# Optimization experiments

Measured on AMD Instinct MI355X. Metric: run time of the kernel, lower is better.

## Reference

```python
import jax, jax.numpy as jnp
import numpy as np

DIM = 1024
HEADS = 16
DK = DIM // HEADS
B, LQ, LKV = 2, 2048, 2048


def setup_inputs() -> dict:
    key = jax.random.key(0)
    ks = jax.random.split(key, 12)
    s = 1.0 / np.sqrt(DIM)
    return {
        "output": jax.random.normal(ks[0], (B, LQ, DIM), jnp.float32),
        "context": jax.random.normal(ks[1], (B, LKV, DIM), jnp.float32),
        # torch nn.Linear(dim, dim): store as [in, out] so y = x @ W + b
        "Wq": jax.random.normal(ks[2], (DIM, DIM), jnp.float32) * s,
        "bq": jax.random.normal(ks[3], (DIM,), jnp.float32) * s,
        "Wk": jax.random.normal(ks[4], (DIM, DIM), jnp.float32) * s,
        "bk": jax.random.normal(ks[5], (DIM,), jnp.float32) * s,
        "Wv": jax.random.normal(ks[6], (DIM, DIM), jnp.float32) * s,
        "bv": jax.random.normal(ks[7], (DIM,), jnp.float32) * s,
        # linear_out: in = 2*dim, out = dim
        "Wo": jax.random.normal(ks[8], (2 * DIM, DIM), jnp.float32) * (1.0 / np.sqrt(2 * DIM)),
        "bo": jax.random.normal(ks[9], (DIM,), jnp.float32) * (1.0 / np.sqrt(2 * DIM)),
    }


def _to_batches(x):
    # [B, L, dim] -> [B*H, L, dk], same layout as the torch reshape/permute
    b, l, _ = x.shape
    return x.reshape(b, l, HEADS, DK).transpose(0, 2, 1, 3).reshape(b * HEADS, l, DK)


def reference(output, context, Wq, bq, Wk, bk, Wv, bv, Wo, bo):
    b, lq, dim = output.shape
    q = _to_batches(output @ Wq + bq)     # [B*H, Lq, dk]
    k = _to_batches(context @ Wk + bk)    # [B*H, Lkv, dk]
    v = _to_batches(context @ Wv + bv)    # [B*H, Lkv, dk]

    scores = jnp.einsum('bqd,bkd->bqk', q, k) / jnp.sqrt(jnp.asarray(DK, q.dtype))
    attn = jax.nn.softmax(scores, axis=-1)            # [B*H, Lq, Lkv]; dropout = identity at eval
    ctx = jnp.einsum('bqk,bkd->bqd', attn, v)          # [B*H, Lq, dk]

    # Faithful to the original (non-standard) reshape:
    # scores.transpose(1,2).contiguous().view(B, -1, dim)
    concat = ctx.transpose(0, 2, 1).reshape(b, -1, dim)  # [B, Lq, dim] (permuted layout)
    combined = jnp.concatenate([concat, output], axis=2)  # [B, Lq, 2*dim]
    out = jnp.tanh(combined @ Wo + bo)                     # [B, Lq, dim]
    return (out, attn)
```

## Files before the change

### kernel.cpp

```cpp
#include <hip/hip_runtime.h>
#include <math.h>
#include <stdint.h>

#define DIM_ 1024
#define HEADS_ 16
#define DK_ 64
#define B_ 2
#define L_ 2048
#define BH_ (B_*HEADS_)
#define M_ (B_*L_)

typedef __attribute__((ext_vector_type(4))) float f32x4;
typedef __attribute__((ext_vector_type(8))) short bf16x8;
typedef __attribute__((ext_vector_type(4))) short bf16x4;

#define QSCALE 0.18033688f

static __device__ __forceinline__ short f2bf(float f) {
    uint32_t u = __builtin_bit_cast(uint32_t, f);
    u += 0x7fffu + ((u >> 16) & 1u);
    return (short)(u >> 16);
}
static __device__ __forceinline__ void gload16(const void* g, void* l) {
    __builtin_amdgcn_global_load_lds(
        (const __attribute__((address_space(1))) unsigned int*)g,
        (__attribute__((address_space(3))) unsigned int*)l, 16, 0, 0);
}

__global__ __launch_bounds__(256)
void prep(const float* __restrict__ xout, const float* __restrict__ xctx,
          const float* __restrict__ Wq, const float* __restrict__ Wk,
          const float* __restrict__ Wv, const float* __restrict__ Wo,
          short* __restrict__ xoutb, short* __restrict__ xctxb,
          short* __restrict__ WqT, short* __restrict__ WkT,
          short* __restrict__ WvT, short* __restrict__ WoT)
{
    __shared__ float ts[64][65];
    const int bid = blockIdx.x;
    const int tid = threadIdx.x;
    if (bid < 4096) {
        const int id = bid * 256 + tid;
        const int nA = (M_ * DIM_) / 8;
        const float* src = (id < nA) ? xout : xctx;
        short* dst = (id < nA) ? xoutb : xctxb;
        const int c = (id < nA) ? id : id - nA;
        const f32x4 v0 = *(const f32x4*)&src[(size_t)c * 8];
        const f32x4 v1 = *(const f32x4*)&src[(size_t)c * 8 + 4];
        bf16x8 o;
#pragma unroll
        for (int i = 0; i < 4; ++i) { o[i] = f2bf(v0[i]); o[4 + i] = f2bf(v1[i]); }
        *(bf16x8*)&dst[(size_t)c * 8] = o;
        return;
    }
    const int flat = bid - 4096;
    const int z = flat >> 9;
    const int rem = flat & 511;
    const int K = (z == 3) ? 2 * DIM_ : DIM_;
    const int k0 = (rem & 31) * 64;
    if (k0 >= K) return;
    const int n0 = (rem >> 5) * 64;
    const float* W = (z == 0) ? Wq : (z == 1) ? Wk : (z == 2) ? Wv : Wo;
    short* WT = (z == 0) ? WqT : (z == 1) ? WkT : (z == 2) ? WvT : WoT;
    {
        const int k = tid >> 2, noff = (tid & 3) * 16;
#pragma unroll
        for (int i = 0; i < 4; ++i)
            *(f32x4*)&ts[k][noff + i * 4] =
                *(const f32x4*)&W[(size_t)(k0 + k) * DIM_ + n0 + noff + i * 4];
    }
    __syncthreads();
    {
        const int n = tid >> 2, koff = (tid & 3) * 16;
#pragma unroll
        for (int c = 0; c < 2; ++c) {
            bf16x8 o;
#pragma unroll
            for (int i = 0; i < 8; ++i) o[i] = f2bf(ts[koff + c * 8 + i][n]);
            *(bf16x8*)&WT[(size_t)(n0 + n) * K + k0 + koff + c * 8] = o;
        }
    }
}

__global__ __launch_bounds__(256)
void qkv_mfma(const short* __restrict__ xoutb, const short* __restrict__ xctxb,
              const short* __restrict__ WqT, const short* __restrict__ WkT,
              const short* __restrict__ WvT,
              const float* __restrict__ bq, const float* __restrict__ bk,
              const float* __restrict__ bv,
              short* __restrict__ qh, short* __restrict__ kh, short* __restrict__ vT)
{
    const int z = blockIdx.z;
    const short* A  = (z == 0) ? xoutb : xctxb;
    const short* Bt = (z == 0) ? WqT : (z == 1) ? WkT : WvT;
    const float* bias = (z == 0) ? bq : (z == 1) ? bk : bv;

    const int flat = blockIdx.y * 8 + blockIdx.x;
    const int wgs = (flat & 7) * 32 + (flat >> 3);
    const int col0 = (wgs & 7) * 128;
    const int row0 = (wgs >> 3) * 128;
    const int tid = threadIdx.x;
    const int lane = tid & 63;
    const int w = tid >> 6;
    const int wm = (w >> 1) * 64, wn = (w & 1) * 64;
    const int l15 = lane & 15, g = lane >> 4;
    const int sub = lane >> 3, slt = lane & 7;

    __shared__ short As[128 * 64];
    __shared__ short Bs[128 * 64];

    const short* pA[4]; const short* pB[4]; short* ldsA[4]; short* ldsB[4];
#pragma unroll
    for (int i = 0; i < 4; ++i) {
        const int r = w * 32 + i * 8 + sub;
        const int sc = ((slt ^ (r & 7)) * 8);
        pA[i] = A  + (size_t)(row0 + r) * DIM_ + sc;
        pB[i] = Bt + (size_t)(col0 + r) * DIM_ + sc;
        ldsA[i] = &As[(w * 32 + i * 8) * 64];
        ldsB[i] = &Bs[(w * 32 + i * 8) * 64];
    }

    f32x4 acc[4][4];
#pragma unroll
    for (int mi = 0; mi < 4; ++mi)
#pragma unroll
        for (int ni = 0; ni < 4; ++ni) acc[mi][ni] = (f32x4)0.f;

    for (int k0 = 0; k0 < DIM_; k0 += 64) {
#pragma unroll
        for (int i = 0; i < 4; ++i) {
            gload16(pA[i] + k0, ldsA[i]);
            gload16(pB[i] + k0, ldsB[i]);
        }
        __syncthreads();
        bf16x8 af[4][2], bfr[4][2];
#pragma unroll
        for (int mi = 0; mi < 4; ++mi) {
            const int wa = wm + mi * 16 + l15;
#pragma unroll
            for (int ks = 0; ks < 2; ++ks)
                af[mi][ks] = *(const bf16x8*)&As[wa * 64 + (((ks * 4 + g) ^ (wa & 7)) * 8)];
        }
#pragma unroll
        for (int ni = 0; ni < 4; ++ni) {
            const int wb = wn + ni * 16 + l15;
#pragma unroll
            for (int ks = 0; ks < 2; ++ks)
                bfr[ni][ks] = *(const bf16x8*)&Bs[wb * 64 + (((ks * 4 + g) ^ (wb & 7)) * 8)];
        }
        __builtin_amdgcn_s_setprio(1);
#pragma unroll
        for (int mi = 0; mi < 4; ++mi)
#pragma unroll
            for (int ni = 0; ni < 4; ++ni)
#pragma unroll
                for (int ks = 0; ks < 2; ++ks)
                    acc[mi][ni] = __builtin_amdgcn_mfma_f32_16x16x32_bf16(af[mi][ks], bfr[ni][ks], acc[mi][ni], 0, 0, 0);
        __builtin_amdgcn_s_setprio(0);
        __syncthreads();
    }

#pragma unroll
    for (int ni = 0; ni < 4; ++ni) {
        const int col = col0 + wn + ni * 16 + l15;
        const int h = col >> 6, dk = col & 63;
        const float bb = bias[col];
#pragma unroll
        for (int mi = 0; mi < 4; ++mi) {
            const int rowb = row0 + wm + mi * 16 + g * 4;
            const int b = rowb >> 11;
            const int l = rowb & (L_ - 1);
            const int bh = b * 16 + h;
            if (z == 2) {
                bf16x4 o;
#pragma unroll
                for (int r = 0; r < 4; ++r) o[r] = f2bf(acc[mi][ni][r] + bb);
                *(bf16x4*)&vT[(size_t)(bh * 64 + dk) * L_ + l] = o;
            } else {
                short* dst = (z == 0) ? qh : kh;
                const float sc = (z == 0) ? QSCALE : 1.0f;
#pragma unroll
                for (int r = 0; r < 4; ++r)
                    dst[((size_t)bh * L_ + l + r) * DK_ + dk] = f2bf((acc[mi][ni][r] + bb) * sc);
            }
        }
    }
}

__global__ __launch_bounds__(512, 8)
void attn_mfma(const short* __restrict__ qh, const short* __restrict__ kh,
               const short* __restrict__ vT,
               float* __restrict__ attn, short* __restrict__ ctxTb)
{
    const int bid = blockIdx.x;
    const int wg = (bid & 7) * 128 + (bid >> 3);
    const int bh = wg >> 5;
    const int q0 = (wg & 31) * 64;

    const int tid = threadIdx.x;
    const int lane = tid & 63;
    const int w = tid >> 6;
    const int wq = w >> 1, wk = w & 1;
    const int l15 = lane & 15, g = lane >> 4;

    __shared__ short SM[17408];
    short* const Kb0 = SM;
    short* const Kb1 = SM + 4096;
    short* const Vb  = SM + 8192;
    short* const Psb = SM + 12288;
    float* const stat = (float*)(SM + 16896);

    const short* kbase = kh + (size_t)bh * (L_ * DK_);
    const short* vbase = vT + (size_t)bh * (DK_ * L_);

    const int lr = lane >> 3, ls = lane & 7;
    const int srow = w * 8 + lr;
    const short* kSrc = kbase + (size_t)srow * DK_ + ((ls ^ (srow & 7)) * 8);
    const short* vSrc = vbase + (size_t)srow * L_ + ((ls ^ (srow & 7)) * 8);

    bf16x8 qf[2];
#pragma unroll
    for (int ks = 0; ks < 2; ++ks)
        qf[ks] = *(const bf16x8*)&qh[((size_t)bh * L_ + q0 + wq * 16 + l15) * DK_ + ks * 32 + g * 8];

    int kbOff[2][2], vbOff[4];
#pragma unroll
    for (int cc = 0; cc < 2; ++cc)
#pragma unroll
        for (int ks = 0; ks < 2; ++ks) {
            const int row = wk * 32 + cc * 16 + l15;
            kbOff[cc][ks] = row * 64 + (((ks * 4 + g) ^ (row & 7)) * 8);
        }
#pragma unroll
    for (int nf = 0; nf < 4; ++nf) {
        const int row = nf * 16 + l15;
        vbOff[nf] = row * 64 + (((wk * 4 + g) ^ (row & 7)) * 8);
    }

    float m[4], s[4];
#pragma unroll
    for (int r = 0; r < 4; ++r) { m[r] = -1e30f; s[r] = 0.f; }

#pragma unroll
    for (int i = 0; i < 3; ++i)
        gload16(kSrc + (size_t)i * 64 * DK_, SM + (i << 12) + w * 512);
    asm volatile("s_waitcnt vmcnt(2)" ::: "memory");
    __builtin_amdgcn_sched_barrier(0);
    __builtin_amdgcn_s_barrier();

    for (int t = 0; t < 32; ++t) {
        if (t < 29)
            gload16(kSrc + (size_t)(t + 3) * 64 * DK_, SM + (((t + 3) & 3) << 12) + w * 512);
        const short* kb = SM + ((t & 3) << 12);
        f32x4 sa[2];
#pragma unroll
        for (int cc = 0; cc < 2; ++cc) sa[cc] = (f32x4)0.f;
        __builtin_amdgcn_s_setprio(1);
#pragma unroll
        for (int cc = 0; cc < 2; ++cc)
#pragma unroll
            for (int ks = 0; ks < 2; ++ks)
                sa[cc] = __builtin_amdgcn_mfma_f32_16x16x32_bf16(qf[ks], *(const bf16x8*)&kb[kbOff[cc][ks]], sa[cc], 0, 0, 0);
        __builtin_amdgcn_s_setprio(0);
#pragma unroll
        for (int r = 0; r < 4; ++r) {
            const float tm = fmaxf(sa[0][r], sa[1][r]);
            const float mn = fmaxf(m[r], tm);
            s[r] = s[r] * exp2f(m[r] - mn) + exp2f(sa[0][r] - mn) + exp2f(sa[1][r] - mn);
            m[r] = mn;
        }
        if (t < 29)       { asm volatile("s_waitcnt vmcnt(2)" ::: "memory"); }
        else if (t == 29) { asm volatile("s_waitcnt vmcnt(1)" ::: "memory"); }
        else if (t == 30) { asm volatile("s_waitcnt vmcnt(0)" ::: "memory"); }
        __builtin_amdgcn_sched_barrier(0);
        if (t < 31) __builtin_amdgcn_s_barrier();
    }
#pragma unroll
    for (int mask = 1; mask <= 8; mask <<= 1) {
#pragma unroll
        for (int r = 0; r < 4; ++r) {
            const float mo = __shfl_xor(m[r], mask);
            const float so = __shfl_xor(s[r], mask);
            const float mn = fmaxf(m[r], mo);
            s[r] = s[r] * exp2f(m[r] - mn) + so * exp2f(mo - mn);
            m[r] = mn;
        }
    }
    if (l15 == 0) {
#pragma unroll
        for (int r = 0; r < 4; ++r) {
            stat[((wq * 2 + wk) * 16 + g * 4 + r) * 2 + 0] = m[r];
            stat[((wq * 2 + wk) * 16 + g * 4 + r) * 2 + 1] = s[r];
        }
    }
    gload16(kSrc, SM + w * 512);
    asm volatile("s_waitcnt lgkmcnt(0)" ::: "memory");
    __builtin_amdgcn_s_barrier();
    float inv_s[4];
#pragma unroll
    for (int r = 0; r < 4; ++r) {
        const float m0 = stat[((wq * 2 + 0) * 16 + g * 4 + r) * 2 + 0];
        const float s0 = stat[((wq * 2 + 0) * 16 + g * 4 + r) * 2 + 1];
        const float m1 = stat[((wq * 2 + 1) * 16 + g * 4 + r) * 2 + 0];
        const float s1 = stat[((wq * 2 + 1) * 16 + g * 4 + r) * 2 + 1];
        const float mn = fmaxf(m0, m1);
        m[r] = mn;
        inv_s[r] = 1.0f / (s0 * exp2f(m0 - mn) + s1 * exp2f(m1 - mn));
    }

    f32x4 cacc[4];
#pragma unroll
    for (int nf = 0; nf < 4; ++nf) cacc[nf] = (f32x4)0.f;

    float* attnB = attn + ((size_t)bh * L_ + q0) * L_;

    asm volatile("s_waitcnt vmcnt(0)" ::: "memory");
    __builtin_amdgcn_sched_barrier(0);
    __builtin_amdgcn_s_barrier();

    for (int t = 0; t < 32; ++t) {
        if (t) {
            asm volatile("s_waitcnt vmcnt(8)" ::: "memory");
            __builtin_amdgcn_sched_barrier(0);
            __builtin_amdgcn_s_barrier();
        }
        gload16(vSrc + t * 64, Vb + w * 512);
        {
            const int tn = (t < 31) ? t + 1 : t;
            gload16(kSrc + (size_t)tn * 64 * DK_, ((t & 1) ? Kb0 : Kb1) + w * 512);
        }
        const short* kb = (t & 1) ? Kb1 : Kb0;
        f32x4 sa[2];
#pragma unroll
        for (int cc = 0; cc < 2; ++cc) sa[cc] = (f32x4)0.f;
        __builtin_amdgcn_s_setprio(1);
#pragma unroll
        for (int cc = 0; cc < 2; ++cc)
#pragma unroll
            for (int ks = 0; ks < 2; ++ks)
                sa[cc] = __builtin_amdgcn_mfma_f32_16x16x32_bf16(qf[ks], *(const bf16x8*)&kb[kbOff[cc][ks]], sa[cc], 0, 0, 0);
        __builtin_amdgcn_s_setprio(0);
#pragma unroll
        for (int cc = 0; cc < 2; ++cc)
#pragma unroll
            for (int r = 0; r < 4; ++r) {
                const float p = exp2f(sa[cc][r] - m[r]) * inv_s[r];
                Psb[(wq * 16 + g * 4 + r) * 72 + wk * 32 + cc * 16 + l15] = f2bf(p);
                __builtin_nontemporal_store(
                    p, attnB + (size_t)(wq * 16 + g * 4 + r) * L_ + t * 64 + wk * 32 + cc * 16 + l15);
            }
        asm volatile("s_waitcnt vmcnt(9) lgkmcnt(0)" ::: "memory");
        __builtin_amdgcn_sched_barrier(0);
        __builtin_amdgcn_s_barrier();
        const bf16x8 pa = *(const bf16x8*)&Psb[(wq * 16 + l15) * 72 + wk * 32 + g * 8];
        __builtin_amdgcn_s_setprio(1);
#pragma unroll
        for (int nf = 0; nf < 4; ++nf)
            cacc[nf] = __builtin_amdgcn_mfma_f32_16x16x32_bf16(pa, *(const bf16x8*)&Vb[vbOff[nf]], cacc[nf], 0, 0, 0);
        __builtin_amdgcn_s_setprio(0);
    }

    __syncthreads();
    float* scr = (float*)Kb0;
    float* scr1 = (float*)Kb1;
    if (wk) {
#pragma unroll
        for (int nf = 0; nf < 4; ++nf) {
            float* p = (nf < 2) ? scr : scr1;
            *(f32x4*)&p[(((wq * 2) + (nf & 1)) * 64 + lane) * 4] = cacc[nf];
        }
    }
    __syncthreads();
    if (!wk) {
#pragma unroll
        for (int nf = 0; nf < 4; ++nf) {
            const float* p = (nf < 2) ? scr : scr1;
            const f32x4 o = cacc[nf] + *(const f32x4*)&p[(((wq * 2) + (nf & 1)) * 64 + lane) * 4];
            bf16x4 ob;
#pragma unroll
            for (int r = 0; r < 4; ++r) ob[r] = f2bf(o[r]);
            *(bf16x4*)&ctxTb[(size_t)(bh * 64 + nf * 16 + l15) * L_ + q0 + wq * 16 + g * 4] = ob;
        }
    }
}

__global__ __launch_bounds__(256)
void out_mfma(const short* __restrict__ ctxTb, const short* __restrict__ xoutb,
              const short* __restrict__ WoT, const float* __restrict__ bo,
              float* __restrict__ out)
{
    const int flat = blockIdx.y * 16 + blockIdx.x;
    const int wgs = (flat & 7) * 64 + (flat >> 3);
    const int col0 = (wgs & 15) * 64;
    const int row0 = (wgs >> 4) * 128;
    const int tid = threadIdx.x;
    const int lane = tid & 63;
    const int w = tid >> 6;
    const int wm = (w >> 1) * 64, wn = (w & 1) * 32;
    const int l15 = lane & 15, g = lane >> 4;
    const int sub = lane >> 3, slt = lane & 7;

    __shared__ short As[128 * 64];
    __shared__ short Bs[64 * 64];

    const short* pA1[4]; const short* pA2[4]; const short* pB[2];
    short* ldsA[4]; short* ldsB[2];
#pragma unroll
    for (int i = 0; i < 4; ++i) {
        const int r = w * 32 + i * 8 + sub;
        const int rr = row0 + r;
        const int b = rr >> 11, l_ = rr & (L_ - 1);
        const int bh = b * 16 + (l_ >> 7), d = (l_ & 127) >> 1;
        const size_t off1 = ((size_t)(bh * 64 + d) << 11) + (size_t)((l_ & 1) << 10);
        const int sc = ((slt ^ (r & 7)) * 8);
        pA1[i] = ctxTb + off1 + sc;
        pA2[i] = xoutb + (size_t)rr * DIM_ + sc;
        ldsA[i] = &As[(w * 32 + i * 8) * 64];
    }
#pragma unroll
    for (int i = 0; i < 2; ++i) {
        const int r = w * 16 + i * 8 + sub;
        const int sc = ((slt ^ (r & 7)) * 8);
        pB[i]  = WoT + (size_t)(col0 + r) * (2 * DIM_) + sc;
        ldsB[i] = &Bs[(w * 16 + i * 8) * 64];
    }

    f32x4 acc[4][2];
#pragma unroll
    for (int mi = 0; mi < 4; ++mi)
#pragma unroll
        for (int ni = 0; ni < 2; ++ni) acc[mi][ni] = (f32x4)0.f;

    for (int k0 = 0; k0 < 2 * DIM_; k0 += 64) {
        const bool first = (k0 < DIM_);
        const int kk = first ? k0 : k0 - DIM_;
#pragma unroll
        for (int i = 0; i < 4; ++i)
            gload16(first ? (pA1[i] + kk) : (pA2[i] + kk), ldsA[i]);
#pragma unroll
        for (int i = 0; i < 2; ++i)
            gload16(pB[i] + k0, ldsB[i]);
        __syncthreads();
        bf16x8 af[4][2], bfr[2][2];
#pragma unroll
        for (int mi = 0; mi < 4; ++mi) {
            const int wa = wm + mi * 16 + l15;
#pragma unroll
            for (int ks = 0; ks < 2; ++ks)
                af[mi][ks] = *(const bf16x8*)&As[wa * 64 + (((ks * 4 + g) ^ (wa & 7)) * 8)];
        }
#pragma unroll
        for (int ni = 0; ni < 2; ++ni) {
            const int wb = wn + ni * 16 + l15;
#pragma unroll
            for (int ks = 0; ks < 2; ++ks)
                bfr[ni][ks] = *(const bf16x8*)&Bs[wb * 64 + (((ks * 4 + g) ^ (wb & 7)) * 8)];
        }
        __builtin_amdgcn_s_setprio(1);
#pragma unroll
        for (int mi = 0; mi < 4; ++mi)
#pragma unroll
            for (int ni = 0; ni < 2; ++ni)
#pragma unroll
                for (int ks = 0; ks < 2; ++ks)
                    acc[mi][ni] = __builtin_amdgcn_mfma_f32_16x16x32_bf16(af[mi][ks], bfr[ni][ks], acc[mi][ni], 0, 0, 0);
        __builtin_amdgcn_s_setprio(0);
        __syncthreads();
    }

#pragma unroll
    for (int ni = 0; ni < 2; ++ni) {
        const int col = col0 + wn + ni * 16 + l15;
        const float bb = bo[col];
#pragma unroll
        for (int mi = 0; mi < 4; ++mi) {
            const int rowb = row0 + wm + mi * 16 + g * 4;
#pragma unroll
            for (int r = 0; r < 4; ++r)
                out[(size_t)(rowb + r) * DIM_ + col] = tanhf(acc[mi][ni][r] + bb);
        }
    }
}

extern "C" void kernel_launch(void* const* d_in, const int* in_sizes, int n_in,
                              void* d_out, int out_size, void* d_ws, size_t ws_size,
                              hipStream_t stream)
{
    const float* xout = (const float*)d_in[0];
    const float* xctx = (const float*)d_in[1];
    const float* Wq = (const float*)d_in[2];
    const float* bq = (const float*)d_in[3];
    const float* Wk = (const float*)d_in[4];
    const float* bk = (const float*)d_in[5];
    const float* Wv = (const float*)d_in[6];
    const float* bv = (const float*)d_in[7];
    const float* Wo = (const float*)d_in[8];
    const float* bo = (const float*)d_in[9];

    float* out  = (float*)d_out;
    float* attn = out + (size_t)M_ * DIM_;

    short* ws = (short*)d_ws;
    short* xoutb = ws;
    short* xctxb = xoutb + (size_t)M_ * DIM_;
    short* WqT   = xctxb + (size_t)M_ * DIM_;
    short* WkT   = WqT + (size_t)DIM_ * DIM_;
    short* WvT   = WkT + (size_t)DIM_ * DIM_;
    short* WoT   = WvT + (size_t)DIM_ * DIM_;
    short* qh    = WoT + (size_t)2 * DIM_ * DIM_;
    short* kh    = qh + (size_t)BH_ * L_ * DK_;
    short* vT    = kh + (size_t)BH_ * L_ * DK_;
    short* ctxTb = vT + (size_t)BH_ * L_ * DK_;

    prep<<<6144, 256, 0, stream>>>(xout, xctx, Wq, Wk, Wv, Wo,
                                   xoutb, xctxb, WqT, WkT, WvT, WoT);
    qkv_mfma<<<dim3(8, 32, 3), 256, 0, stream>>>(
        xoutb, xctxb, WqT, WkT, WvT, bq, bk, bv, qh, kh, vT);
    attn_mfma<<<1024, 512, 0, stream>>>(qh, kh, vT, attn, ctxTb);
    out_mfma<<<dim3(16, 32), 256, 0, stream>>>(ctxTb, xoutb, WoT, bo, out);
}
```

Measured before the change: 279.2 us.

## Process two K tiles per barrier and lazily rescale softmax running max

The softmax statistics pass now handles two 64-row K tiles per loop iteration and loads the next pair together, which halves the number of workgroup barriers and waitcnt points. The running max is only updated, with its exp2 rescale of the sum, when some lane's tile max exceeds the current max by more than 8 in the log2 domain. Otherwise the new exponentials are added straight to the sum. The re-prefetch of the first K tile is moved after the barrier that follows the stat writes. The trade-off is a shorter effective prefetch distance, because each iteration waits on vmcnt(0) for the pair it just issued, plus a wave-wide vote branch in the inner loop.

```diff
diff --git a/kernel.cpp b/kernel.cpp
--- a/kernel.cpp
+++ b/kernel.cpp
@@ -241,38 +241,58 @@
     for (int r = 0; r < 4; ++r) { m[r] = -1e30f; s[r] = 0.f; }
 
 #pragma unroll
-    for (int i = 0; i < 3; ++i)
+    for (int i = 0; i < 4; ++i)
         gload16(kSrc + (size_t)i * 64 * DK_, SM + (i << 12) + w * 512);
     asm volatile("s_waitcnt vmcnt(2)" ::: "memory");
     __builtin_amdgcn_sched_barrier(0);
     __builtin_amdgcn_s_barrier();
 
-    for (int t = 0; t < 32; ++t) {
-        if (t < 29)
-            gload16(kSrc + (size_t)(t + 3) * 64 * DK_, SM + (((t + 3) & 3) << 12) + w * 512);
-        const short* kb = SM + ((t & 3) << 12);
-        f32x4 sa[2];
-#pragma unroll
-        for (int cc = 0; cc < 2; ++cc) sa[cc] = (f32x4)0.f;
-        __builtin_amdgcn_s_setprio(1);
-#pragma unroll
-        for (int cc = 0; cc < 2; ++cc)
-#pragma unroll
-            for (int ks = 0; ks < 2; ++ks)
-                sa[cc] = __builtin_amdgcn_mfma_f32_16x16x32_bf16(qf[ks], *(const bf16x8*)&kb[kbOff[cc][ks]], sa[cc], 0, 0, 0);
-        __builtin_amdgcn_s_setprio(0);
-#pragma unroll
-        for (int r = 0; r < 4; ++r) {
-            const float tm = fmaxf(sa[0][r], sa[1][r]);
-            const float mn = fmaxf(m[r], tm);
-            s[r] = s[r] * exp2f(m[r] - mn) + exp2f(sa[0][r] - mn) + exp2f(sa[1][r] - mn);
-            m[r] = mn;
-        }
-        if (t < 29)       { asm volatile("s_waitcnt vmcnt(2)" ::: "memory"); }
-        else if (t == 29) { asm volatile("s_waitcnt vmcnt(1)" ::: "memory"); }
-        else if (t == 30) { asm volatile("s_waitcnt vmcnt(0)" ::: "memory"); }
-        __builtin_amdgcn_sched_barrier(0);
-        if (t < 31) __builtin_amdgcn_s_barrier();
+    for (int j = 0; j < 16; ++j) {
+        if (j >= 1 && j < 15) {
+            const size_t t2 = (size_t)(2 * j + 2);
+            gload16(kSrc + t2 * 64 * DK_, SM + (((2 * j + 2) & 3) << 12) + w * 512);
+            gload16(kSrc + (t2 + 1) * 64 * DK_, SM + (((2 * j + 3) & 3) << 12) + w * 512);
+        }
+        f32x4 sa[2][2];
+#pragma unroll
+        for (int u = 0; u < 2; ++u) {
+            const short* kb = SM + (((2 * j + u) & 3) << 12);
+            sa[u][0] = (f32x4)0.f; sa[u][1] = (f32x4)0.f;
+            __builtin_amdgcn_s_setprio(1);
+#pragma unroll
+            for (int cc = 0; cc < 2; ++cc)
+#pragma unroll
+                for (int ks = 0; ks < 2; ++ks)
+                    sa[u][cc] = __builtin_amdgcn_mfma_f32_16x16x32_bf16(qf[ks], *(const bf16x8*)&kb[kbOff[cc][ks]], sa[u][cc], 0, 0, 0);
+            __builtin_amdgcn_s_setprio(0);
+        }
+#pragma unroll
+        for (int u = 0; u < 2; ++u) {
+            float tm[4];
+            bool need = false;
+#pragma unroll
+            for (int r = 0; r < 4; ++r) {
+                tm[r] = fmaxf(sa[u][0][r], sa[u][1][r]);
+                need |= (tm[r] > m[r] + 8.0f);
+            }
+            if (__any(need)) {
+#pragma unroll
+                for (int r = 0; r < 4; ++r) {
+                    const float mn = fmaxf(m[r], tm[r]);
+                    s[r] = s[r] * exp2f(m[r] - mn) + exp2f(sa[u][0][r] - mn) + exp2f(sa[u][1][r] - mn);
+                    m[r] = mn;
+                }
+            } else {
+#pragma unroll
+                for (int r = 0; r < 4; ++r)
+                    s[r] += exp2f(sa[u][0][r] - m[r]) + exp2f(sa[u][1][r] - m[r]);
+            }
+        }
+        if (j < 15) {
+            asm volatile("s_waitcnt vmcnt(0)" ::: "memory");
+            __builtin_amdgcn_sched_barrier(0);
+            __builtin_amdgcn_s_barrier();
+        }
     }
 #pragma unroll
     for (int mask = 1; mask <= 8; mask <<= 1) {
@@ -292,9 +312,9 @@
             stat[((wq * 2 + wk) * 16 + g * 4 + r) * 2 + 1] = s[r];
         }
     }
-    gload16(kSrc, SM + w * 512);
     asm volatile("s_waitcnt lgkmcnt(0)" ::: "memory");
     __builtin_amdgcn_s_barrier();
+    gload16(kSrc, SM + w * 512);
     float inv_s[4];
 #pragma unroll
     for (int r = 0; r < 4; ++r) {
```

Measured after the change: 284.6 us. About the same (+2.0%).

## Load K/V fragments directly from global into registers, dropping LDS staging and barriers

Applied to the files above, without the earlier changes.

The attention kernel no longer stages K and V tiles through shared memory with async global-to-LDS copies and block-wide barriers. Each wave now reads its own MFMA operand fragments straight from global memory into registers, with a two-deep register double buffer in the stats pass. The P tile exchange is kept wave-local, so the per-iteration s_barrier is removed and the occupancy hint in launch_bounds is relaxed. This trades barrier and LDS-copy overhead for redundant global or cache reads, since several waves now fetch the same K rows, and for higher register pressure and exposed load latency.

```diff
diff --git a/kernel.cpp b/kernel.cpp
--- a/kernel.cpp
+++ b/kernel.cpp
@@ -186,7 +186,7 @@
     }
 }
 
-__global__ __launch_bounds__(512, 8)
+__global__ __launch_bounds__(512)
 void attn_mfma(const short* __restrict__ qh, const short* __restrict__ kh,
                const short* __restrict__ vT,
                float* __restrict__ attn, short* __restrict__ ctxTb)
@@ -203,76 +203,87 @@
     const int l15 = lane & 15, g = lane >> 4;
 
     __shared__ short SM[17408];
-    short* const Kb0 = SM;
-    short* const Kb1 = SM + 4096;
-    short* const Vb  = SM + 8192;
     short* const Psb = SM + 12288;
     float* const stat = (float*)(SM + 16896);
 
     const short* kbase = kh + (size_t)bh * (L_ * DK_);
     const short* vbase = vT + (size_t)bh * (DK_ * L_);
 
-    const int lr = lane >> 3, ls = lane & 7;
-    const int srow = w * 8 + lr;
-    const short* kSrc = kbase + (size_t)srow * DK_ + ((ls ^ (srow & 7)) * 8);
-    const short* vSrc = vbase + (size_t)srow * L_ + ((ls ^ (srow & 7)) * 8);
-
     bf16x8 qf[2];
 #pragma unroll
     for (int ks = 0; ks < 2; ++ks)
         qf[ks] = *(const bf16x8*)&qh[((size_t)bh * L_ + q0 + wq * 16 + l15) * DK_ + ks * 32 + g * 8];
 
-    int kbOff[2][2], vbOff[4];
+    int kfOff[2][2], vfOff[4];
 #pragma unroll
     for (int cc = 0; cc < 2; ++cc)
 #pragma unroll
-        for (int ks = 0; ks < 2; ++ks) {
-            const int row = wk * 32 + cc * 16 + l15;
-            kbOff[cc][ks] = row * 64 + (((ks * 4 + g) ^ (row & 7)) * 8);
-        }
-#pragma unroll
-    for (int nf = 0; nf < 4; ++nf) {
-        const int row = nf * 16 + l15;
-        vbOff[nf] = row * 64 + (((wk * 4 + g) ^ (row & 7)) * 8);
-    }
+        for (int ks = 0; ks < 2; ++ks)
+            kfOff[cc][ks] = (wk * 32 + cc * 16 + l15) * 64 + ks * 32 + g * 8;
+#pragma unroll
+    for (int nf = 0; nf < 4; ++nf)
+        vfOff[nf] = (nf * 16 + l15) * L_ + wk * 32 + g * 8;
 
     float m[4], s[4];
 #pragma unroll
     for (int r = 0; r < 4; ++r) { m[r] = -1e30f; s[r] = 0.f; }
 
-#pragma unroll
-    for (int i = 0; i < 3; ++i)
-        gload16(kSrc + (size_t)i * 64 * DK_, SM + (i << 12) + w * 512);
-    asm volatile("s_waitcnt vmcnt(2)" ::: "memory");
-    __builtin_amdgcn_sched_barrier(0);
-    __builtin_amdgcn_s_barrier();
-
-    for (int t = 0; t < 32; ++t) {
-        if (t < 29)
-            gload16(kSrc + (size_t)(t + 3) * 64 * DK_, SM + (((t + 3) & 3) << 12) + w * 512);
-        const short* kb = SM + ((t & 3) << 12);
-        f32x4 sa[2];
-#pragma unroll
-        for (int cc = 0; cc < 2; ++cc) sa[cc] = (f32x4)0.f;
-        __builtin_amdgcn_s_setprio(1);
-#pragma unroll
-        for (int cc = 0; cc < 2; ++cc)
-#pragma unroll
-            for (int ks = 0; ks < 2; ++ks)
-                sa[cc] = __builtin_amdgcn_mfma_f32_16x16x32_bf16(qf[ks], *(const bf16x8*)&kb[kbOff[cc][ks]], sa[cc], 0, 0, 0);
-        __builtin_amdgcn_s_setprio(0);
-#pragma unroll
-        for (int r = 0; r < 4; ++r) {
-            const float tm = fmaxf(sa[0][r], sa[1][r]);
-            const float mn = fmaxf(m[r], tm);
-            s[r] = s[r] * exp2f(m[r] - mn) + exp2f(sa[0][r] - mn) + exp2f(sa[1][r] - mn);
-            m[r] = mn;
-        }
-        if (t < 29)       { asm volatile("s_waitcnt vmcnt(2)" ::: "memory"); }
-        else if (t == 29) { asm volatile("s_waitcnt vmcnt(1)" ::: "memory"); }
-        else if (t == 30) { asm volatile("s_waitcnt vmcnt(0)" ::: "memory"); }
-        __builtin_amdgcn_sched_barrier(0);
-        if (t < 31) __builtin_amdgcn_s_barrier();
+    bf16x8 kA[2][2], kB[2][2];
+#pragma unroll
+    for (int cc = 0; cc < 2; ++cc)
+#pragma unroll
+        for (int ks = 0; ks < 2; ++ks)
+            kA[cc][ks] = *(const bf16x8*)&kbase[kfOff[cc][ks]];
+
+    for (int t = 0; t < 32; t += 2) {
+        if (t + 1 < 32) {
+            const short* kt = kbase + (size_t)(t + 1) * 64 * DK_;
+#pragma unroll
+            for (int cc = 0; cc < 2; ++cc)
+#pragma unroll
+                for (int ks = 0; ks < 2; ++ks)
+                    kB[cc][ks] = *(const bf16x8*)&kt[kfOff[cc][ks]];
+        }
+        {
+            f32x4 sa0 = (f32x4)0.f, sa1 = (f32x4)0.f;
+            __builtin_amdgcn_s_setprio(1);
+            sa0 = __builtin_amdgcn_mfma_f32_16x16x32_bf16(qf[0], kA[0][0], sa0, 0, 0, 0);
+            sa0 = __builtin_amdgcn_mfma_f32_16x16x32_bf16(qf[1], kA[0][1], sa0, 0, 0, 0);
+            sa1 = __builtin_amdgcn_mfma_f32_16x16x32_bf16(qf[0], kA[1][0], sa1, 0, 0, 0);
+            sa1 = __builtin_amdgcn_mfma_f32_16x16x32_bf16(qf[1], kA[1][1], sa1, 0, 0, 0);
+            __builtin_amdgcn_s_setprio(0);
+#pragma unroll
+            for (int r = 0; r < 4; ++r) {
+                const float tm = fmaxf(sa0[r], sa1[r]);
+                const float mn = fmaxf(m[r], tm);
+                s[r] = s[r] * exp2f(m[r] - mn) + exp2f(sa0[r] - mn) + exp2f(sa1[r] - mn);
+                m[r] = mn;
+            }
+        }
+        if (t + 2 < 32) {
+            const short* kt = kbase + (size_t)(t + 2) * 64 * DK_;
+#pragma unroll
+            for (int cc = 0; cc < 2; ++cc)
+#pragma unroll
+                for (int ks = 0; ks < 2; ++ks)
+                    kA[cc][ks] = *(const bf16x8*)&kt[kfOff[cc][ks]];
+        }
+        {
+            f32x4 sa0 = (f32x4)0.f, sa1 = (f32x4)0.f;
+            __builtin_amdgcn_s_setprio(1);
+            sa0 = __builtin_amdgcn_mfma_f32_16x16x32_bf16(qf[0], kB[0][0], sa0, 0, 0, 0);
+            sa0 = __builtin_amdgcn_mfma_f32_16x16x32_bf16(qf[1], kB[0][1], sa0, 0, 0, 0);
+            sa1 = __builtin_amdgcn_mfma_f32_16x16x32_bf16(qf[0], kB[1][0], sa1, 0, 0, 0);
+            sa1 = __builtin_amdgcn_mfma_f32_16x16x32_bf16(qf[1], kB[1][1], sa1, 0, 0, 0);
+            __builtin_amdgcn_s_setprio(0);
+#pragma unroll
+            for (int r = 0; r < 4; ++r) {
+                const float tm = fmaxf(sa0[r], sa1[r]);
+                const float mn = fmaxf(m[r], tm);
+                s[r] = s[r] * exp2f(m[r] - mn) + exp2f(sa0[r] - mn) + exp2f(sa1[r] - mn);
+                m[r] = mn;
+            }
+        }
     }
 #pragma unroll
     for (int mask = 1; mask <= 8; mask <<= 1) {
@@ -292,9 +303,7 @@
             stat[((wq * 2 + wk) * 16 + g * 4 + r) * 2 + 1] = s[r];
         }
     }
-    gload16(kSrc, SM + w * 512);
-    asm volatile("s_waitcnt lgkmcnt(0)" ::: "memory");
-    __builtin_amdgcn_s_barrier();
+    __syncthreads();
     float inv_s[4];
 #pragma unroll
     for (int r = 0; r < 4; ++r) {
@@ -312,56 +321,54 @@
     for (int nf = 0; nf < 4; ++nf) cacc[nf] = (f32x4)0.f;
 
     float* attnB = attn + ((size_t)bh * L_ + q0) * L_;
-
-    asm volatile("s_waitcnt vmcnt(0)" ::: "memory");
-    __builtin_amdgcn_sched_barrier(0);
-    __builtin_amdgcn_s_barrier();
+    short* const psW = &Psb[(wq * 16 + g * 4) * 72 + wk * 32 + l15];
+    const short* const psR = &Psb[(wq * 16 + l15) * 72 + wk * 32 + g * 8];
 
     for (int t = 0; t < 32; ++t) {
-        if (t) {
-            asm volatile("s_waitcnt vmcnt(8)" ::: "memory");
-            __builtin_amdgcn_sched_barrier(0);
-            __builtin_amdgcn_s_barrier();
-        }
-        gload16(vSrc + t * 64, Vb + w * 512);
-        {
-            const int tn = (t < 31) ? t + 1 : t;
-            gload16(kSrc + (size_t)tn * 64 * DK_, ((t & 1) ? Kb0 : Kb1) + w * 512);
-        }
-        const short* kb = (t & 1) ? Kb1 : Kb0;
-        f32x4 sa[2];
-#pragma unroll
-        for (int cc = 0; cc < 2; ++cc) sa[cc] = (f32x4)0.f;
+        const short* kt = kbase + (size_t)t * 64 * DK_;
+        const short* vt = vbase + t * 64;
+        bf16x8 kf00, kf01, kf10, kf11, vf0, vf1, vf2, vf3;
+        kf00 = *(const bf16x8*)&kt[kfOff[0][0]];
+        kf01 = *(const bf16x8*)&kt[kfOff[0][1]];
+        kf10 = *(const bf16x8*)&kt[kfOff[1][0]];
+        kf11 = *(const bf16x8*)&kt[kfOff[1][1]];
+        vf0 = *(const bf16x8*)&vt[vfOff[0]];
+        vf1 = *(const bf16x8*)&vt[vfOff[1]];
+        vf2 = *(const bf16x8*)&vt[vfOff[2]];
+        vf3 = *(const bf16x8*)&vt[vfOff[3]];
+
+        f32x4 sa0 = (f32x4)0.f, sa1 = (f32x4)0.f;
         __builtin_amdgcn_s_setprio(1);
-#pragma unroll
-        for (int cc = 0; cc < 2; ++cc)
-#pragma unroll
-            for (int ks = 0; ks < 2; ++ks)
-                sa[cc] = __builtin_amdgcn_mfma_f32_16x16x32_bf16(qf[ks], *(const bf16x8*)&kb[kbOff[cc][ks]], sa[cc], 0, 0, 0);
+        sa0 = __builtin_amdgcn_mfma_f32_16x16x32_bf16(qf[0], kf00, sa0, 0, 0, 0);
+        sa0 = __builtin_amdgcn_mfma_f32_16x16x32_bf16(qf[1], kf01, sa0, 0, 0, 0);
+        sa1 = __builtin_amdgcn_mfma_f32_16x16x32_bf16(qf[0], kf10, sa1, 0, 0, 0);
+        sa1 = __builtin_amdgcn_mfma_f32_16x16x32_bf16(qf[1], kf11, sa1, 0, 0, 0);
         __builtin_amdgcn_s_setprio(0);
-#pragma unroll
-        for (int cc = 0; cc < 2; ++cc)
-#pragma unroll
-            for (int r = 0; r < 4; ++r) {
-                const float p = exp2f(sa[cc][r] - m[r]) * inv_s[r];
-                Psb[(wq * 16 + g * 4 + r) * 72 + wk * 32 + cc * 16 + l15] = f2bf(p);
-                __builtin_nontemporal_store(
-                    p, attnB + (size_t)(wq * 16 + g * 4 + r) * L_ + t * 64 + wk * 32 + cc * 16 + l15);
-            }
-        asm volatile("s_waitcnt vmcnt(9) lgkmcnt(0)" ::: "memory");
+
+        float* aB = attnB + (size_t)(wq * 16 + g * 4) * L_ + t * 64 + wk * 32 + l15;
+#pragma unroll
+        for (int r = 0; r < 4; ++r) {
+            const float p0 = exp2f(sa0[r] - m[r]) * inv_s[r];
+            const float p1 = exp2f(sa1[r] - m[r]) * inv_s[r];
+            psW[r * 72 + 0]  = f2bf(p0);
+            psW[r * 72 + 16] = f2bf(p1);
+            __builtin_nontemporal_store(p0, aB + (size_t)r * L_);
+            __builtin_nontemporal_store(p1, aB + (size_t)r * L_ + 16);
+        }
+        asm volatile("s_waitcnt lgkmcnt(0)" ::: "memory");
         __builtin_amdgcn_sched_barrier(0);
-        __builtin_amdgcn_s_barrier();
-        const bf16x8 pa = *(const bf16x8*)&Psb[(wq * 16 + l15) * 72 + wk * 32 + g * 8];
+        const bf16x8 pa = *(const bf16x8*)psR;
         __builtin_amdgcn_s_setprio(1);
-#pragma unroll
-        for (int nf = 0; nf < 4; ++nf)
-            cacc[nf] = __builtin_amdgcn_mfma_f32_16x16x32_bf16(pa, *(const bf16x8*)&Vb[vbOff[nf]], cacc[nf], 0, 0, 0);
+        cacc[0] = __builtin_amdgcn_mfma_f32_16x16x32_bf16(pa, vf0, cacc[0], 0, 0, 0);
+        cacc[1] = __builtin_amdgcn_mfma_f32_16x16x32_bf16(pa, vf1, cacc[1], 0, 0, 0);
+        cacc[2] = __builtin_amdgcn_mfma_f32_16x16x32_bf16(pa, vf2, cacc[2], 0, 0, 0);
+        cacc[3] = __builtin_amdgcn_mfma_f32_16x16x32_bf16(pa, vf3, cacc[3], 0, 0, 0);
         __builtin_amdgcn_s_setprio(0);
     }
 
     __syncthreads();
-    float* scr = (float*)Kb0;
-    float* scr1 = (float*)Kb1;
+    float* scr = (float*)SM;
+    float* scr1 = (float*)(SM + 4096);
     if (wk) {
 #pragma unroll
         for (int nf = 0; nf < 4; ++nf) {
```

Measured after the change: 443.3 us. 1.59x slower.

## Double-buffer V tiles, swizzle P scratch, drop mid-iteration barrier in attention

Applied to the files above, without the earlier changes.

V tiles now get a second LDS buffer. The next K and V tiles are prefetched together one step ahead, so the PV MFMA no longer waits on a V load issued in the same iteration. The probability scratch uses an XOR-swizzled 128-byte row layout, which is meant to avoid LDS bank conflicts. The workgroup barrier between writing P and reading it is replaced by a per-wave lgkmcnt wait, which is valid because each wave reads only the P it wrote itself. LDS use per block grows, and this may reduce occupancy.

```diff
diff --git a/kernel.cpp b/kernel.cpp
--- a/kernel.cpp
+++ b/kernel.cpp
@@ -202,12 +202,13 @@
     const int wq = w >> 1, wk = w & 1;
     const int l15 = lane & 15, g = lane >> 4;
 
-    __shared__ short SM[17408];
+    __shared__ short SM[20480];
     short* const Kb0 = SM;
     short* const Kb1 = SM + 4096;
-    short* const Vb  = SM + 8192;
-    short* const Psb = SM + 12288;
-    float* const stat = (float*)(SM + 16896);
+    short* const Vb0 = SM + 8192;
+    short* const Vb1 = SM + 12288;
+    char*  const PsB = (char*)(SM + 16384);
+    float* const stat = (float*)(SM + 16384);
 
     const short* kbase = kh + (size_t)bh * (L_ * DK_);
     const short* vbase = vT + (size_t)bh * (DK_ * L_);
@@ -235,6 +236,10 @@
         const int row = nf * 16 + l15;
         vbOff[nf] = row * 64 + (((wk * 4 + g) ^ (row & 7)) * 8);
     }
+    const int psW0 = (wq * 16 + g * 4) * 128;
+    const int psWc = (wk * 32 + l15) * 2;
+    const int psRrow = wq * 16 + l15;
+    const int psRaddr = psRrow * 128 + (((wk * 64 + g * 16)) ^ ((psRrow & 7) << 4));
 
     float m[4], s[4];
 #pragma unroll
@@ -292,7 +297,8 @@
             stat[((wq * 2 + wk) * 16 + g * 4 + r) * 2 + 1] = s[r];
         }
     }
-    gload16(kSrc, SM + w * 512);
+    gload16(kSrc, Kb0 + w * 512);
+    gload16(vSrc, Vb0 + w * 512);
     asm volatile("s_waitcnt lgkmcnt(0)" ::: "memory");
     __builtin_amdgcn_s_barrier();
     float inv_s[4];
@@ -323,12 +329,12 @@
             __builtin_amdgcn_sched_barrier(0);
             __builtin_amdgcn_s_barrier();
         }
-        gload16(vSrc + t * 64, Vb + w * 512);
-        {
-            const int tn = (t < 31) ? t + 1 : t;
-            gload16(kSrc + (size_t)tn * 64 * DK_, ((t & 1) ? Kb0 : Kb1) + w * 512);
+        if (t < 31) {
+            gload16(kSrc + (size_t)(t + 1) * 64 * DK_, ((t & 1) ? Kb0 : Kb1) + w * 512);
+            gload16(vSrc + (t + 1) * 64, ((t & 1) ? Vb0 : Vb1) + w * 512);
         }
         const short* kb = (t & 1) ? Kb1 : Kb0;
+        const short* vb = (t & 1) ? Vb1 : Vb0;
         f32x4 sa[2];
 #pragma unroll
         for (int cc = 0; cc < 2; ++cc) sa[cc] = (f32x4)0.f;
@@ -344,18 +350,18 @@
 #pragma unroll
             for (int r = 0; r < 4; ++r) {
                 const float p = exp2f(sa[cc][r] - m[r]) * inv_s[r];
-                Psb[(wq * 16 + g * 4 + r) * 72 + wk * 32 + cc * 16 + l15] = f2bf(p);
+                const int rrow = wq * 16 + g * 4 + r;
+                *(short*)(PsB + rrow * 128 + (((psWc + cc * 32)) ^ ((rrow & 7) << 4))) = f2bf(p);
                 __builtin_nontemporal_store(
-                    p, attnB + (size_t)(wq * 16 + g * 4 + r) * L_ + t * 64 + wk * 32 + cc * 16 + l15);
+                    p, attnB + (size_t)rrow * L_ + t * 64 + wk * 32 + cc * 16 + l15);
             }
-        asm volatile("s_waitcnt vmcnt(9) lgkmcnt(0)" ::: "memory");
+        asm volatile("s_waitcnt lgkmcnt(0)" ::: "memory");
         __builtin_amdgcn_sched_barrier(0);
-        __builtin_amdgcn_s_barrier();
-        const bf16x8 pa = *(const bf16x8*)&Psb[(wq * 16 + l15) * 72 + wk * 32 + g * 8];
+        const bf16x8 pa = *(const bf16x8*)(PsB + psRaddr);
         __builtin_amdgcn_s_setprio(1);
 #pragma unroll
         for (int nf = 0; nf < 4; ++nf)
-            cacc[nf] = __builtin_amdgcn_mfma_f32_16x16x32_bf16(pa, *(const bf16x8*)&Vb[vbOff[nf]], cacc[nf], 0, 0, 0);
+            cacc[nf] = __builtin_amdgcn_mfma_f32_16x16x32_bf16(pa, *(const bf16x8*)&vb[vbOff[nf]], cacc[nf], 0, 0, 0);
         __builtin_amdgcn_s_setprio(0);
     }
 
```

After: 302.6 us. 1.08x slower.
